# Optimization experiments

Hardware: AMD Instinct MI355X
Metric: run time of the kernel (lower is better)

Reference implementation:

```python
import jax, jax.numpy as jnp
import numpy as np

B, L, DM, H = 2, 2048, 512, 8
D = DM // H
FACTOR = 5
NUM_K = int(FACTOR * np.ceil(np.log(L)))  # 40
NUM_Q = NUM_K  # q_len == k_len here
EPS = 1e-5


def setup_inputs() -> dict:
    key = jax.random.key(0)
    ks = jax.random.split(key, 12)
    s = DM ** -0.5
    return {
        "q": jax.random.normal(ks[0], (B, L, DM), jnp.float32),
        "k": jax.random.normal(ks[1], (B, L, DM), jnp.float32),
        "v": jax.random.normal(ks[2], (B, L, DM), jnp.float32),
        "Wq": jax.random.normal(ks[3], (DM, DM), jnp.float32) * s,
        "bq": jnp.zeros((DM,), jnp.float32),
        "Wk": jax.random.normal(ks[4], (DM, DM), jnp.float32) * s,
        "bk": jnp.zeros((DM,), jnp.float32),
        "Wv": jax.random.normal(ks[5], (DM, DM), jnp.float32) * s,
        "bv": jnp.zeros((DM,), jnp.float32),
        "gamma": jnp.ones((DM,), jnp.float32),
        "beta": jnp.zeros((DM,), jnp.float32),
        "random_index": jax.random.randint(ks[6], (L, NUM_K), 0, L, jnp.int32),
    }


def _heads(x):
    # [B, L, DM] -> [B, H, L, D]
    return x.reshape(B, L, H, D).transpose(0, 2, 1, 3)


def reference(q, k, v, Wq, bq, Wk, bk, Wv, bv, gamma, beta, random_index):
    qp = _heads(q @ Wq + bq)
    kp = _heads(k @ Wk + bk)
    vp = _heads(v @ Wv + bv)

    # ProbSparse: sample NUM_K keys per query position (shared over batch/head)
    k_samp = kp[:, :, random_index, :]                      # [B,H,L,NUM_K,D]
    pre = jnp.einsum('bhid,bhijd->bhij', qp, k_samp)        # [B,H,L,NUM_K]
    measure = pre.max(-1) - pre.sum(-1) / L                 # sparsity measure [B,H,L]
    _, q_idx = jax.lax.top_k(measure, NUM_Q)                # [B,H,NUM_Q]

    q_sel = jnp.take_along_axis(qp, q_idx[..., None], axis=2)   # [B,H,NUM_Q,D]
    attn = jnp.einsum('bhid,bhjd->bhij', q_sel, kp) * D ** -0.5 # [B,H,NUM_Q,L]
    attn = jax.nn.softmax(attn, axis=-1)                    # dropout = identity (eval)
    out_sel = jnp.einsum('bhij,bhjd->bhid', attn, vp)       # [B,H,NUM_Q,D]

    # use_mask=False path: context is the mean of v over keys
    v_mean = vp.mean(axis=2)                                # [B,H,D]
    context = jnp.broadcast_to(v_mean[:, :, None, :], (B, H, L, D))
    bi = jnp.arange(B)[:, None, None]
    hi = jnp.arange(H)[None, :, None]
    out = context.at[bi, hi, q_idx].set(out_sel)            # scatter selected rows

    out = out.transpose(0, 2, 1, 3).reshape(B, L, DM)
    y = out + q
    mu = y.mean(-1, keepdims=True)
    var = y.var(-1, keepdims=True)
    yn = (y - mu) / jnp.sqrt(var + EPS) * gamma + beta
    return (yn, attn)
```

## Files before the change

kernel.cpp:

```cpp
#include <hip/hip_runtime.h>
#include <math.h>

#define BB 2
#define LL 2048
#define DMM 512
#define HH 8
#define DD 64
#define NUMK 40
#define NUMQ 40
#define LNEPS 1e-5f
#define LSEG 512
#define NLS 4

typedef unsigned short ushort_t;
typedef __attribute__((ext_vector_type(8))) short bf16x8;
typedef __attribute__((ext_vector_type(4))) float f32x4;

__device__ inline ushort_t f2bf(float x) {
    union { float f; unsigned int u; } v; v.f = x;
    unsigned int r = v.u + 0x7fffu + ((v.u >> 16) & 1u);
    return (ushort_t)(r >> 16);
}
__device__ inline float bf2f(ushort_t h) {
    union { unsigned int u; float f; } v; v.u = ((unsigned int)h) << 16;
    return v.f;
}

__global__ __launch_bounds__(256) void convert_x_kernel(
    const float* __restrict__ q, const float* __restrict__ k, const float* __restrict__ v,
    ushort_t* __restrict__ Xh, ushort_t* __restrict__ Xl) {
    const size_t plane = (size_t)BB * LL * DMM;
    const float* X = (blockIdx.y == 0) ? q : (blockIdx.y == 1) ? k : v;
    ushort_t* xh = Xh + plane * blockIdx.y;
    ushort_t* xl = Xl + plane * blockIdx.y;
    const size_t base = ((size_t)blockIdx.x * 256 + threadIdx.x) * 8;
    float4 a = *(const float4*)(X + base);
    float4 b = *(const float4*)(X + base + 4);
    float xs[8] = {a.x, a.y, a.z, a.w, b.x, b.y, b.z, b.w};
    unsigned int hp[4], lp[4];
#pragma unroll
    for (int j = 0; j < 4; ++j) {
        ushort_t h0 = f2bf(xs[2 * j]),     h1 = f2bf(xs[2 * j + 1]);
        ushort_t l0 = f2bf(xs[2 * j] - bf2f(h0));
        ushort_t l1 = f2bf(xs[2 * j + 1] - bf2f(h1));
        hp[j] = (unsigned int)h0 | ((unsigned int)h1 << 16);
        lp[j] = (unsigned int)l0 | ((unsigned int)l1 << 16);
    }
    *(uint4*)(xh + base) = make_uint4(hp[0], hp[1], hp[2], hp[3]);
    *(uint4*)(xl + base) = make_uint4(lp[0], lp[1], lp[2], lp[3]);
}

__global__ __launch_bounds__(256) void convert_w_kernel(
    const float* __restrict__ Wq, const float* __restrict__ Wk, const float* __restrict__ Wv,
    ushort_t* __restrict__ Wht, ushort_t* __restrict__ Wlt) {
    __shared__ float tile[64][65];
    const size_t plane = (size_t)DMM * DMM;
    const float* W = (blockIdx.z == 0) ? Wq : (blockIdx.z == 1) ? Wk : Wv;
    ushort_t* wht = Wht + plane * blockIdx.z;
    ushort_t* wlt = Wlt + plane * blockIdx.z;
    const int n0 = blockIdx.x * 64, k0 = blockIdx.y * 64;
    const int t = threadIdx.x;
    const int d = t & 63, g = t >> 6;
    for (int rr = g; rr < 64; rr += 4)
        tile[rr][d] = W[(size_t)(k0 + rr) * DMM + n0 + d];
    __syncthreads();
    for (int cc = g; cc < 64; cc += 4) {
        float x = tile[d][cc];
        ushort_t hi = f2bf(x);
        ushort_t lo = f2bf(x - bf2f(hi));
        wht[(size_t)(n0 + cc) * DMM + k0 + d] = hi;
        wlt[(size_t)(n0 + cc) * DMM + k0 + d] = lo;
    }
}

__device__ inline void stage_one(const ushort_t* __restrict__ g, ushort_t* lbuf,
                                 int r0, int lane, int k0) {
    const int r = r0 + (lane >> 3);
    const int c = (lane & 7) ^ (r & 7);
    const ushort_t* gp = g + (size_t)r * DMM + k0 + c * 8;
    __builtin_amdgcn_global_load_lds(
        (const __attribute__((address_space(1))) unsigned int*)gp,
        (__attribute__((address_space(3))) unsigned int*)(lbuf + (size_t)r0 * 64),
        16, 0, 0);
}
__device__ inline bf16x8 frag_ld(const ushort_t* buf, int row, int c) {
    const int idx = row * 8 + (c ^ (row & 7));
    return *(const bf16x8*)(buf + idx * 8);
}

__global__ __launch_bounds__(256, 2) void proj_mfma_kernel(
    const ushort_t* __restrict__ Xh, const ushort_t* __restrict__ Xl,
    const ushort_t* __restrict__ Wht, const ushort_t* __restrict__ Wlt,
    const float* __restrict__ bq, const float* __restrict__ bk, const float* __restrict__ bv,
    float* __restrict__ Oq, float* __restrict__ Ok, float* __restrict__ Ov) {
    const int z = blockIdx.z;
    const size_t xplane = (size_t)BB * LL * DMM;
    const size_t wplane = (size_t)DMM * DMM;
    const ushort_t* ah_g = Xh + xplane * z;
    const ushort_t* al_g = Xl + xplane * z;
    const ushort_t* bh_g = Wht + wplane * z;
    const ushort_t* bl_g = Wlt + wplane * z;
    const float* bias = (z == 0) ? bq : (z == 1) ? bk : bv;
    float* Out = (z == 0) ? Oq : (z == 1) ? Ok : Ov;

    __shared__ __align__(16) ushort_t bufAh[128 * 64];
    __shared__ __align__(16) ushort_t bufAl[128 * 64];
    __shared__ __align__(16) ushort_t bufBh[128 * 64];
    __shared__ __align__(16) ushort_t bufBl[128 * 64];

    const int t = threadIdx.x;
    const int lane = t & 63, w = t >> 6;
    const int wm = (w & 1) * 64, wn = (w >> 1) * 64;
    const int m0 = blockIdx.x * 128, j0 = blockIdx.y * 128;

    const ushort_t* A_h = ah_g + (size_t)m0 * DMM;
    const ushort_t* A_l = al_g + (size_t)m0 * DMM;
    const ushort_t* B_h = bh_g + (size_t)j0 * DMM;
    const ushort_t* B_l = bl_g + (size_t)j0 * DMM;

    f32x4 acc[4][4];
#pragma unroll
    for (int i = 0; i < 4; ++i)
#pragma unroll
        for (int j = 0; j < 4; ++j) acc[i][j] = (f32x4){0.f, 0.f, 0.f, 0.f};

    for (int ch = 0; ch < 8; ++ch) {
        const int k0 = ch * 64;
#pragma unroll
        for (int i = 0; i < 4; ++i) {
            const int r0 = (w * 4 + i) * 8;
            stage_one(A_h, bufAh, r0, lane, k0);
            stage_one(A_l, bufAl, r0, lane, k0);
            stage_one(B_h, bufBh, r0, lane, k0);
            stage_one(B_l, bufBl, r0, lane, k0);
        }
        __syncthreads();
#pragma unroll
        for (int ks = 0; ks < 2; ++ks) {
            const int cc = ks * 4 + (lane >> 4);
            bf16x8 fah[4], fal[4];
#pragma unroll
            for (int tm = 0; tm < 4; ++tm) {
                const int row = wm + tm * 16 + (lane & 15);
                fah[tm] = frag_ld(bufAh, row, cc);
                fal[tm] = frag_ld(bufAl, row, cc);
            }
#pragma unroll
            for (int tn = 0; tn < 4; ++tn) {
                const int rowb = wn + tn * 16 + (lane & 15);
                const bf16x8 fbh = frag_ld(bufBh, rowb, cc);
                const bf16x8 fbl = frag_ld(bufBl, rowb, cc);
#pragma unroll
                for (int tm = 0; tm < 4; ++tm) {
                    acc[tm][tn] = __builtin_amdgcn_mfma_f32_16x16x32_bf16(fah[tm], fbh, acc[tm][tn], 0, 0, 0);
                    acc[tm][tn] = __builtin_amdgcn_mfma_f32_16x16x32_bf16(fal[tm], fbh, acc[tm][tn], 0, 0, 0);
                    acc[tm][tn] = __builtin_amdgcn_mfma_f32_16x16x32_bf16(fah[tm], fbl, acc[tm][tn], 0, 0, 0);
                }
            }
        }
        __syncthreads();
    }

#pragma unroll
    for (int tn = 0; tn < 4; ++tn) {
        const int gn = j0 + wn + tn * 16 + (lane & 15);
        const float bvv = bias[gn];
        const int h = gn >> 6, d = gn & 63;
#pragma unroll
        for (int tm = 0; tm < 4; ++tm) {
#pragma unroll
            for (int reg = 0; reg < 4; ++reg) {
                const int gm = m0 + wm + tm * 16 + (lane >> 4) * 4 + reg;
                const int b = gm >> 11, l = gm & (LL - 1);
                Out[(((size_t)(b * HH + h)) * LL + l) * DD + d] = acc[tm][tn][reg] + bvv;
            }
        }
    }
}

__global__ __launch_bounds__(256) void measure_kernel(const float* __restrict__ qp2,
                                                      const float* __restrict__ kp2,
                                                      const int* __restrict__ rnd,
                                                      float* __restrict__ measure) {
    const int t = threadIdx.x;
    const int lane = t & 63;
    const int wv = t >> 6;
    const int g = lane >> 4;
    const int dq = (lane & 15) * 4;
    const int bh = blockIdx.x;
    const int i = blockIdx.y * 16 + wv * 4 + g;
    const float4 qv = *(const float4*)(qp2 + ((size_t)bh * LL + i) * DD + dq);
    const float* kbase = kp2 + (size_t)bh * LL * DD;
    const int* rp = rnd + i * NUMK;
    float mx = -INFINITY, sm = 0.f;
#pragma unroll 8
    for (int j = 0; j < NUMK; ++j) {
        const int row = rp[j];
        const float4 kv = *(const float4*)(kbase + (size_t)row * DD + dq);
        float p = kv.x * qv.x;
        p = fmaf(kv.y, qv.y, p); p = fmaf(kv.z, qv.z, p); p = fmaf(kv.w, qv.w, p);
        p += __shfl_xor(p, 1, 64);
        p += __shfl_xor(p, 2, 64);
        p += __shfl_xor(p, 4, 64);
        p += __shfl_xor(p, 8, 64);
        mx = fmaxf(mx, p);
        sm += p;
    }
    if ((lane & 15) == 0) measure[(size_t)bh * LL + i] = mx - sm * (1.0f / LL);
}

__global__ __launch_bounds__(256) void topk_kernel(const float* __restrict__ measure,
                                                   int* __restrict__ q_idx,
                                                   int* __restrict__ sel_pos) {
    __shared__ unsigned int keys[LL];
    __shared__ int hist[256];
    __shared__ unsigned int prefix_sh;
    __shared__ int need_sh;
    __shared__ unsigned int cval[256];
    __shared__ int cidx[256];
    __shared__ int cnt;
    const int t = threadIdx.x;
    const int bh = blockIdx.x;
    for (int i = t; i < LL; i += 256) {
        const float f = measure[(size_t)bh * LL + i];
        unsigned int u = __float_as_uint(f);
        keys[i] = (u & 0x80000000u) ? ~u : (u | 0x80000000u);
        sel_pos[(size_t)bh * LL + i] = -1;
    }
    if (t == 0) { prefix_sh = 0u; need_sh = NUMQ; cnt = 0; }
    __syncthreads();

    for (int round = 0; round < 4; ++round) {
        const int shift = 24 - round * 8;
        hist[t] = 0;
        __syncthreads();
        const unsigned int pref = prefix_sh;
        const unsigned int mask = (round == 0) ? 0u : (0xFFFFFFFFu << (shift + 8));
        for (int i = t; i < LL; i += 256) {
            const unsigned int key = keys[i];
            if ((key & mask) == pref)
                atomicAdd(&hist[(key >> shift) & 0xFF], 1);
        }
        __syncthreads();
        if (t == 0) {
            const int need = need_sh;
            int acc = 0;
            int v = 255;
            for (; v > 0; --v) {
                if (acc + hist[v] >= need) break;
                acc += hist[v];
            }
            need_sh = need - acc;
            prefix_sh = pref | ((unsigned int)v << shift);
        }
        __syncthreads();
    }
    const unsigned int K40 = prefix_sh;

    for (int i = t; i < LL; i += 256) {
        if (keys[i] >= K40) {
            int p = atomicAdd(&cnt, 1);
            if (p < 256) { cval[p] = keys[i]; cidx[p] = i; }
        }
    }
    __syncthreads();
    int M = cnt; if (M > 256) M = 256;
    for (int i = t; i < M; i += 256) {
        const unsigned int ki = cval[i];
        const int ii = cidx[i];
        int r = 0;
        for (int j = 0; j < M; ++j) {
            const unsigned int kj = cval[j];
            r += (kj > ki || (kj == ki && cidx[j] < ii)) ? 1 : 0;
        }
        if (r < NUMQ) {
            q_idx[bh * NUMQ + r] = ii;
            sel_pos[(size_t)bh * LL + ii] = r;
        }
    }
}

__global__ __launch_bounds__(256) void attn_part_kernel(
    const float* __restrict__ qp2, const float* __restrict__ kp2,
    const float* __restrict__ vp2, const int* __restrict__ q_idx,
    float* __restrict__ attn_out, float* __restrict__ part_m,
    float* __restrict__ part_s, float* __restrict__ part_pv) {
    __shared__ __align__(16) float buf[2][64 * 64];
    __shared__ __align__(16) float sc[4][LSEG];
    __shared__ float pvred[16][68];
    const int t = threadIdx.x;
    const int lane = t & 63, w = t >> 6;
    const int bh = blockIdx.x;
    const int qg = blockIdx.y;
    const int ls = blockIdx.z;
    const int l0 = ls * LSEG;
    const int dseg = lane >> 4;
    const int kk = lane & 15;

    float qrf[4][16];
#pragma unroll
    for (int qq = 0; qq < 4; ++qq) {
        const int qi = q_idx[bh * NUMQ + qg * 4 + qq];
        const float* qrow = qp2 + ((size_t)bh * LL + qi) * DD + dseg * 16;
#pragma unroll
        for (int j = 0; j < 4; ++j) {
            float4 v = *(const float4*)(qrow + j * 4);
            qrf[qq][j * 4 + 0] = v.x * 0.125f;
            qrf[qq][j * 4 + 1] = v.y * 0.125f;
            qrf[qq][j * 4 + 2] = v.z * 0.125f;
            qrf[qq][j * 4 + 3] = v.w * 0.125f;
        }
    }

    const float* kseg = kp2 + ((size_t)bh * LL + l0) * DD;
    const float* vseg = vp2 + ((size_t)bh * LL + l0) * DD;

    auto stage = [&](const float* gsrc, float* lb) {
#pragma unroll
        for (int i = 0; i < 4; ++i) {
            const int instr = w * 4 + i;
            const int r = instr * 4 + (lane >> 4);
            const int cg = (lane & 15) ^ (r & 15);
            const float* gp = gsrc + (size_t)r * DD + cg * 4;
            __builtin_amdgcn_global_load_lds(
                (const __attribute__((address_space(1))) unsigned int*)gp,
                (__attribute__((address_space(3))) unsigned int*)(lb + instr * 256),
                16, 0, 0);
        }
    };

    stage(kseg, buf[0]);
    const int krow = w * 16 + kk;
    for (int c = 0; c < 8; ++c) {
        __syncthreads();
        if (c < 7) stage(kseg + (size_t)(c + 1) * 64 * DD, buf[(c + 1) & 1]);
        const float* lb = buf[c & 1];
        float dot[4] = {0.f, 0.f, 0.f, 0.f};
#pragma unroll
        for (int j = 0; j < 4; ++j) {
            const int cg = dseg * 4 + j;
            const float4 k4 = *(const float4*)(lb + krow * 64 + ((cg ^ (krow & 15)) * 4));
            const float kf[4] = {k4.x, k4.y, k4.z, k4.w};
#pragma unroll
            for (int qq = 0; qq < 4; ++qq)
#pragma unroll
                for (int m = 0; m < 4; ++m)
                    dot[qq] = fmaf(qrf[qq][j * 4 + m], kf[m], dot[qq]);
        }
#pragma unroll
        for (int qq = 0; qq < 4; ++qq) {
            dot[qq] += __shfl_xor(dot[qq], 16, 64);
            dot[qq] += __shfl_xor(dot[qq], 32, 64);
        }
        const float sel = (dseg == 0) ? dot[0] : (dseg == 1) ? dot[1]
                        : (dseg == 2) ? dot[2] : dot[3];
        sc[dseg][c * 64 + krow] = sel;
    }
    stage(vseg, buf[0]);
    __syncthreads();

    const int row = bh * NUMQ + qg * 4 + w;
    {
        float* srow = sc[w];
        float4 v0 = *(float4*)(srow + lane * 8);
        float4 v1 = *(float4*)(srow + lane * 8 + 4);
        float m = fmaxf(fmaxf(fmaxf(v0.x, v0.y), fmaxf(v0.z, v0.w)),
                        fmaxf(fmaxf(v1.x, v1.y), fmaxf(v1.z, v1.w)));
#pragma unroll
        for (int off = 32; off > 0; off >>= 1) m = fmaxf(m, __shfl_xor(m, off, 64));
        v0.x = __expf(v0.x - m); v0.y = __expf(v0.y - m);
        v0.z = __expf(v0.z - m); v0.w = __expf(v0.w - m);
        v1.x = __expf(v1.x - m); v1.y = __expf(v1.y - m);
        v1.z = __expf(v1.z - m); v1.w = __expf(v1.w - m);
        *(float4*)(srow + lane * 8) = v0;
        *(float4*)(srow + lane * 8 + 4) = v1;
        float* arow = attn_out + (size_t)row * LL + l0;
        *(float4*)(arow + lane * 8) = v0;
        *(float4*)(arow + lane * 8 + 4) = v1;
        float s = (v0.x + v0.y + v0.z + v0.w) + (v1.x + v1.y + v1.z + v1.w);
#pragma unroll
        for (int off = 32; off > 0; off >>= 1) s += __shfl_xor(s, off, 64);
        if (lane == 0) {
            part_m[row * NLS + ls] = m;
            part_s[row * NLS + ls] = s;
        }
    }

    const int dq4 = (t & 15) * 4;
    const int grp = t >> 4;
    float4 acc[4];
#pragma unroll
    for (int qq = 0; qq < 4; ++qq) acc[qq] = make_float4(0.f, 0.f, 0.f, 0.f);
    for (int c = 0; c < 8; ++c) {
        __syncthreads();
        if (c < 7) stage(vseg + (size_t)(c + 1) * 64 * DD, buf[(c + 1) & 1]);
        const float* lb = buf[c & 1];
        float pa[4][4];
#pragma unroll
        for (int qq = 0; qq < 4; ++qq)
            *(float4*)&pa[qq][0] = *(const float4*)&sc[qq][c * 64 + grp * 4];
#pragma unroll
        for (int i = 0; i < 4; ++i) {
            const int r = grp * 4 + i;
            const float4 v4 = *(const float4*)(lb + r * 64 + (((t & 15) ^ (r & 15)) * 4));
#pragma unroll
            for (int qq = 0; qq < 4; ++qq) {
                acc[qq].x = fmaf(pa[qq][i], v4.x, acc[qq].x);
                acc[qq].y = fmaf(pa[qq][i], v4.y, acc[qq].y);
                acc[qq].z = fmaf(pa[qq][i], v4.z, acc[qq].z);
                acc[qq].w = fmaf(pa[qq][i], v4.w, acc[qq].w);
            }
        }
    }
#pragma unroll
    for (int qq = 0; qq < 4; ++qq) {
        __syncthreads();
        *(float4*)&pvred[grp][dq4] = acc[qq];
        __syncthreads();
        if (t < DD) {
            float s = 0.f;
#pragma unroll
            for (int u = 0; u < 16; ++u) s += pvred[u][t];
            const int prow = bh * NUMQ + qg * 4 + qq;
            part_pv[((size_t)prow * NLS + ls) * DD + t] = s;
        }
    }
}

__global__ __launch_bounds__(256) void attn_fin_kernel(
    const float* __restrict__ part_m, const float* __restrict__ part_s,
    const float* __restrict__ part_pv, float* __restrict__ attn_out,
    float* __restrict__ out_sel) {
    const int row = blockIdx.x;
    const int t = threadIdx.x;
    float m0 = part_m[row * NLS + 0], m1 = part_m[row * NLS + 1];
    float m2 = part_m[row * NLS + 2], m3 = part_m[row * NLS + 3];
    float M = fmaxf(fmaxf(m0, m1), fmaxf(m2, m3));
    float f[NLS];
    f[0] = __expf(m0 - M); f[1] = __expf(m1 - M);
    f[2] = __expf(m2 - M); f[3] = __expf(m3 - M);
    float T = part_s[row * NLS + 0] * f[0] + part_s[row * NLS + 1] * f[1]
            + part_s[row * NLS + 2] * f[2] + part_s[row * NLS + 3] * f[3];
    const float inv = 1.0f / T;
    float* arow = attn_out + (size_t)row * LL;
    {
        float4 v0 = *(const float4*)&arow[4 * t];
        float4 v1 = *(const float4*)&arow[1024 + 4 * t];
        const float g0 = f[(4 * t) >> 9] * inv;
        const float g1 = f[(1024 + 4 * t) >> 9] * inv;
        v0.x *= g0; v0.y *= g0; v0.z *= g0; v0.w *= g0;
        v1.x *= g1; v1.y *= g1; v1.z *= g1; v1.w *= g1;
        *(float4*)&arow[4 * t] = v0;
        *(float4*)&arow[1024 + 4 * t] = v1;
    }
    if (t < DD) {
        float s = part_pv[((size_t)row * NLS + 0) * DD + t] * f[0]
                + part_pv[((size_t)row * NLS + 1) * DD + t] * f[1]
                + part_pv[((size_t)row * NLS + 2) * DD + t] * f[2]
                + part_pv[((size_t)row * NLS + 3) * DD + t] * f[3];
        out_sel[(size_t)row * DD + t] = s * inv;
    }
}

__global__ __launch_bounds__(256) void vmean1_kernel(const float* __restrict__ vp2,
                                                     float* __restrict__ partial) {
    __shared__ float pv[256];
    const int t = threadIdx.x;
    const int chunk = blockIdx.x & 31;
    const int bh = blockIdx.x >> 5;
    const int d = t & 63, g = t >> 6;
    const int l0 = chunk * 64;
    float acc = 0.f;
    for (int l = l0 + g; l < l0 + 64; l += 4)
        acc += vp2[((size_t)bh * LL + l) * DD + d];
    pv[t] = acc;
    __syncthreads();
    if (t < 64)
        partial[(size_t)blockIdx.x * 64 + t] = pv[t] + pv[64 + t] + pv[128 + t] + pv[192 + t];
}

__global__ __launch_bounds__(64) void vmean2_kernel(const float* __restrict__ partial,
                                                    float* __restrict__ v_mean) {
    const int bh = blockIdx.x;
    const int t = threadIdx.x;
    float s = 0.f;
    for (int c = 0; c < 32; ++c)
        s += partial[((size_t)bh * 32 + c) * 64 + t];
    v_mean[bh * 64 + t] = s * (1.0f / LL);
}

__global__ __launch_bounds__(512) void final_kernel(const float* __restrict__ q_in,
                                                    const int* __restrict__ sel_pos,
                                                    const float* __restrict__ out_sel,
                                                    const float* __restrict__ v_mean,
                                                    const float* __restrict__ gamma,
                                                    const float* __restrict__ beta,
                                                    float* __restrict__ yout) {
    __shared__ float wred[8];
    const int j = threadIdx.x;
    const int lane = j & 63, wv = j >> 6;
    const int tok = blockIdx.x;
    const int b = tok >> 11;
    const int l = tok & (LL - 1);
    const int h = wv, d = lane;
    const int bh = b * HH + h;
    const int p = sel_pos[(size_t)bh * LL + l];
    float val = (p >= 0) ? out_sel[((size_t)bh * NUMQ + p) * DD + d]
                         : v_mean[bh * DD + d];
    float y = val + q_in[(size_t)tok * DMM + j];
    float s = y;
#pragma unroll
    for (int off = 32; off > 0; off >>= 1) s += __shfl_xor(s, off, 64);
    if (lane == 0) wred[wv] = s;
    __syncthreads();
    float tot = 0.f;
#pragma unroll
    for (int u = 0; u < 8; ++u) tot += wred[u];
    float mu = tot * (1.0f / DMM);
    __syncthreads();
    float dv = y - mu;
    float s2 = dv * dv;
#pragma unroll
    for (int off = 32; off > 0; off >>= 1) s2 += __shfl_xor(s2, off, 64);
    if (lane == 0) wred[wv] = s2;
    __syncthreads();
    float tot2 = 0.f;
#pragma unroll
    for (int u = 0; u < 8; ++u) tot2 += wred[u];
    float var = tot2 * (1.0f / DMM);
    float yn = dv * rsqrtf(var + LNEPS) * gamma[j] + beta[j];
    yout[(size_t)tok * DMM + j] = yn;
}

extern "C" void kernel_launch(void* const* d_in, const int* in_sizes, int n_in,
                              void* d_out, int out_size, void* d_ws, size_t ws_size,
                              hipStream_t stream) {
    const float* q     = (const float*)d_in[0];
    const float* k     = (const float*)d_in[1];
    const float* v     = (const float*)d_in[2];
    const float* Wq    = (const float*)d_in[3];
    const float* bq    = (const float*)d_in[4];
    const float* Wk    = (const float*)d_in[5];
    const float* bk    = (const float*)d_in[6];
    const float* Wv    = (const float*)d_in[7];
    const float* bv    = (const float*)d_in[8];
    const float* gamma = (const float*)d_in[9];
    const float* beta  = (const float*)d_in[10];
    const int*   rnd   = (const int*)d_in[11];

    float* ws = (float*)d_ws;
    const size_t proj_sz = (size_t)BB * HH * LL * DD;
    float* qp2     = ws;
    float* kp2     = qp2 + proj_sz;
    float* vp2     = kp2 + proj_sz;
    float* measure = vp2 + proj_sz;
    float* out_sel = measure + (size_t)BB * HH * LL;
    float* v_mean  = out_sel + (size_t)BB * HH * NUMQ * DD;
    float* partial = v_mean + (size_t)BB * HH * DD;
    float* part_m  = partial + (size_t)BB * HH * 32 * 64;
    float* part_s  = part_m + (size_t)BB * HH * NUMQ * NLS;
    float* part_pv = part_s + (size_t)BB * HH * NUMQ * NLS;
    int*   q_idx   = (int*)(part_pv + (size_t)BB * HH * NUMQ * NLS * DD);
    int*   sel_pos = q_idx + BB * HH * NUMQ;
    ushort_t* Xh  = (ushort_t*)(sel_pos + BB * HH * LL);
    ushort_t* Xl  = Xh + 3 * proj_sz;
    ushort_t* Wht = Xl + 3 * proj_sz;
    ushort_t* Wlt = Wht + 3 * (size_t)DMM * DMM;

    float* yn_out   = (float*)d_out;
    float* attn_out = yn_out + (size_t)BB * LL * DMM;

    convert_x_kernel<<<dim3(BB * LL * DMM / (256 * 8), 3), 256, 0, stream>>>(q, k, v, Xh, Xl);
    convert_w_kernel<<<dim3(DMM / 64, DMM / 64, 3), 256, 0, stream>>>(Wq, Wk, Wv, Wht, Wlt);
    proj_mfma_kernel<<<dim3(BB * LL / 128, DMM / 128, 3), 256, 0, stream>>>(
        Xh, Xl, Wht, Wlt, bq, bk, bv, qp2, kp2, vp2);
    vmean1_kernel<<<BB * HH * 32, 256, 0, stream>>>(vp2, partial);
    vmean2_kernel<<<BB * HH, 64, 0, stream>>>(partial, v_mean);
    measure_kernel<<<dim3(BB * HH, LL / 16), 256, 0, stream>>>(qp2, kp2, rnd, measure);
    topk_kernel<<<BB * HH, 256, 0, stream>>>(measure, q_idx, sel_pos);
    attn_part_kernel<<<dim3(BB * HH, NUMQ / 4, NLS), 256, 0, stream>>>(
        qp2, kp2, vp2, q_idx, attn_out, part_m, part_s, part_pv);
    attn_fin_kernel<<<BB * HH * NUMQ, 256, 0, stream>>>(
        part_m, part_s, part_pv, attn_out, out_sel);
    final_kernel<<<BB * LL, 512, 0, stream>>>(q, sel_pos, out_sel, v_mean, gamma, beta, yn_out);
}
```

Before: 217.9 us.

## Restructure attention partials so each block handles all queries over shorter key segments

The attention partial kernel now processes all 40 selected queries per block over 128-key segments (16 segments), staging K and V once into LDS and reusing them across every query. Before, it used 4-query groups over 512-key segments, so K and V were reloaded ten times per head. The finalize kernel is generalized to merge 16 partials. Separately, the projection GEMM grid is flattened into one dimension with a remapped block order, which may improve L2 locality across the XCDs. The cost is more partial results to merge and larger LDS use per block.

```diff
diff --git a/kernel.cpp b/kernel.cpp
--- a/kernel.cpp
+++ b/kernel.cpp
@@ -9,8 +9,8 @@
 #define NUMK 40
 #define NUMQ 40
 #define LNEPS 1e-5f
-#define LSEG 512
-#define NLS 4
+#define LSEG 128
+#define NLS 16
 
 typedef unsigned short ushort_t;
 typedef __attribute__((ext_vector_type(8))) short bf16x8;
@@ -93,7 +93,10 @@
     const ushort_t* __restrict__ Wht, const ushort_t* __restrict__ Wlt,
     const float* __restrict__ bq, const float* __restrict__ bk, const float* __restrict__ bv,
     float* __restrict__ Oq, float* __restrict__ Ok, float* __restrict__ Ov) {
-    const int z = blockIdx.z;
+    const int orig = blockIdx.x;
+    const int c = (orig & 7) * 48 + (orig >> 3);
+    const int jb = c & 3, mb = (c >> 2) & 31, z = c >> 7;
+
     const size_t xplane = (size_t)BB * LL * DMM;
     const size_t wplane = (size_t)DMM * DMM;
     const ushort_t* ah_g = Xh + xplane * z;
@@ -111,7 +114,7 @@
     const int t = threadIdx.x;
     const int lane = t & 63, w = t >> 6;
     const int wm = (w & 1) * 64, wn = (w >> 1) * 64;
-    const int m0 = blockIdx.x * 128, j0 = blockIdx.y * 128;
+    const int m0 = mb * 128, j0 = jb * 128;
 
     const ushort_t* A_h = ah_g + (size_t)m0 * DMM;
     const ushort_t* A_l = al_g + (size_t)m0 * DMM;
@@ -285,145 +288,126 @@
     const float* __restrict__ vp2, const int* __restrict__ q_idx,
     float* __restrict__ attn_out, float* __restrict__ part_m,
     float* __restrict__ part_s, float* __restrict__ part_pv) {
-    __shared__ __align__(16) float buf[2][64 * 64];
-    __shared__ __align__(16) float sc[4][LSEG];
-    __shared__ float pvred[16][68];
+    __shared__ __align__(16) float Qs[NUMQ][68];
+    __shared__ __align__(16) float Ks[LSEG * 64];
+    __shared__ __align__(16) float Vs[LSEG * 64];
+    __shared__ __align__(16) float Ss[NUMQ][136];
     const int t = threadIdx.x;
     const int lane = t & 63, w = t >> 6;
     const int bh = blockIdx.x;
-    const int qg = blockIdx.y;
-    const int ls = blockIdx.z;
+    const int ls = blockIdx.y;
     const int l0 = ls * LSEG;
-    const int dseg = lane >> 4;
-    const int kk = lane & 15;
-
-    float qrf[4][16];
-#pragma unroll
-    for (int qq = 0; qq < 4; ++qq) {
-        const int qi = q_idx[bh * NUMQ + qg * 4 + qq];
-        const float* qrow = qp2 + ((size_t)bh * LL + qi) * DD + dseg * 16;
-#pragma unroll
-        for (int j = 0; j < 4; ++j) {
-            float4 v = *(const float4*)(qrow + j * 4);
-            qrf[qq][j * 4 + 0] = v.x * 0.125f;
-            qrf[qq][j * 4 + 1] = v.y * 0.125f;
-            qrf[qq][j * 4 + 2] = v.z * 0.125f;
-            qrf[qq][j * 4 + 3] = v.w * 0.125f;
-        }
+
+    for (int idx = t; idx < NUMQ * 16; idx += 256) {
+        const int r = idx >> 4, c4 = idx & 15;
+        const int qi = q_idx[bh * NUMQ + r];
+        float4 v = *(const float4*)(qp2 + ((size_t)bh * LL + qi) * DD + c4 * 4);
+        Qs[r][c4 * 4 + 0] = v.x * 0.125f;
+        Qs[r][c4 * 4 + 1] = v.y * 0.125f;
+        Qs[r][c4 * 4 + 2] = v.z * 0.125f;
+        Qs[r][c4 * 4 + 3] = v.w * 0.125f;
     }
 
     const float* kseg = kp2 + ((size_t)bh * LL + l0) * DD;
     const float* vseg = vp2 + ((size_t)bh * LL + l0) * DD;
-
-    auto stage = [&](const float* gsrc, float* lb) {
-#pragma unroll
-        for (int i = 0; i < 4; ++i) {
-            const int instr = w * 4 + i;
-            const int r = instr * 4 + (lane >> 4);
-            const int cg = (lane & 15) ^ (r & 15);
-            const float* gp = gsrc + (size_t)r * DD + cg * 4;
-            __builtin_amdgcn_global_load_lds(
-                (const __attribute__((address_space(1))) unsigned int*)gp,
-                (__attribute__((address_space(3))) unsigned int*)(lb + instr * 256),
-                16, 0, 0);
-        }
-    };
-
-    stage(kseg, buf[0]);
-    const int krow = w * 16 + kk;
-    for (int c = 0; c < 8; ++c) {
-        __syncthreads();
-        if (c < 7) stage(kseg + (size_t)(c + 1) * 64 * DD, buf[(c + 1) & 1]);
-        const float* lb = buf[c & 1];
-        float dot[4] = {0.f, 0.f, 0.f, 0.f};
-#pragma unroll
-        for (int j = 0; j < 4; ++j) {
-            const int cg = dseg * 4 + j;
-            const float4 k4 = *(const float4*)(lb + krow * 64 + ((cg ^ (krow & 15)) * 4));
-            const float kf[4] = {k4.x, k4.y, k4.z, k4.w};
-#pragma unroll
-            for (int qq = 0; qq < 4; ++qq)
-#pragma unroll
-                for (int m = 0; m < 4; ++m)
-                    dot[qq] = fmaf(qrf[qq][j * 4 + m], kf[m], dot[qq]);
-        }
-#pragma unroll
-        for (int qq = 0; qq < 4; ++qq) {
-            dot[qq] += __shfl_xor(dot[qq], 16, 64);
-            dot[qq] += __shfl_xor(dot[qq], 32, 64);
-        }
-        const float sel = (dseg == 0) ? dot[0] : (dseg == 1) ? dot[1]
-                        : (dseg == 2) ? dot[2] : dot[3];
-        sc[dseg][c * 64 + krow] = sel;
-    }
-    stage(vseg, buf[0]);
-    __syncthreads();
-
-    const int row = bh * NUMQ + qg * 4 + w;
-    {
-        float* srow = sc[w];
-        float4 v0 = *(float4*)(srow + lane * 8);
-        float4 v1 = *(float4*)(srow + lane * 8 + 4);
-        float m = fmaxf(fmaxf(fmaxf(v0.x, v0.y), fmaxf(v0.z, v0.w)),
-                        fmaxf(fmaxf(v1.x, v1.y), fmaxf(v1.z, v1.w)));
-#pragma unroll
-        for (int off = 32; off > 0; off >>= 1) m = fmaxf(m, __shfl_xor(m, off, 64));
-        v0.x = __expf(v0.x - m); v0.y = __expf(v0.y - m);
-        v0.z = __expf(v0.z - m); v0.w = __expf(v0.w - m);
-        v1.x = __expf(v1.x - m); v1.y = __expf(v1.y - m);
-        v1.z = __expf(v1.z - m); v1.w = __expf(v1.w - m);
-        *(float4*)(srow + lane * 8) = v0;
-        *(float4*)(srow + lane * 8 + 4) = v1;
-        float* arow = attn_out + (size_t)row * LL + l0;
-        *(float4*)(arow + lane * 8) = v0;
-        *(float4*)(arow + lane * 8 + 4) = v1;
-        float s = (v0.x + v0.y + v0.z + v0.w) + (v1.x + v1.y + v1.z + v1.w);
-#pragma unroll
-        for (int off = 32; off > 0; off >>= 1) s += __shfl_xor(s, off, 64);
-        if (lane == 0) {
+#pragma unroll
+    for (int i = 0; i < 8; ++i) {
+        const int r0 = (w * 8 + i) * 4;
+        const int r = r0 + (lane >> 4);
+        const int cg = (lane & 15) ^ (r & 15);
+        __builtin_amdgcn_global_load_lds(
+            (const __attribute__((address_space(1))) unsigned int*)(kseg + (size_t)r * DD + cg * 4),
+            (__attribute__((address_space(3))) unsigned int*)(Ks + r0 * 64), 16, 0, 0);
+        __builtin_amdgcn_global_load_lds(
+            (const __attribute__((address_space(1))) unsigned int*)(vseg + (size_t)r * DD + cg * 4),
+            (__attribute__((address_space(3))) unsigned int*)(Vs + r0 * 64), 16, 0, 0);
+    }
+    __syncthreads();
+
+    const int qt = t >> 5;
+    const int jt = t & 31;
+    float acc[5][4];
+#pragma unroll
+    for (int i = 0; i < 5; ++i)
+#pragma unroll
+        for (int jj = 0; jj < 4; ++jj) acc[i][jj] = 0.f;
+
+    for (int c4 = 0; c4 < 16; ++c4) {
+        float4 q4[5];
+#pragma unroll
+        for (int i = 0; i < 5; ++i)
+            q4[i] = *(const float4*)&Qs[qt + 8 * i][c4 * 4];
+#pragma unroll
+        for (int jj = 0; jj < 4; ++jj) {
+            const int r = jt + 32 * jj;
+            const float4 k4 = *(const float4*)&Ks[r * 64 + ((c4 ^ (r & 15)) * 4)];
+#pragma unroll
+            for (int i = 0; i < 5; ++i) {
+                acc[i][jj] = fmaf(q4[i].x, k4.x, acc[i][jj]);
+                acc[i][jj] = fmaf(q4[i].y, k4.y, acc[i][jj]);
+                acc[i][jj] = fmaf(q4[i].z, k4.z, acc[i][jj]);
+                acc[i][jj] = fmaf(q4[i].w, k4.w, acc[i][jj]);
+            }
+        }
+    }
+
+#pragma unroll
+    for (int i = 0; i < 5; ++i) {
+        const int r = qt + 8 * i;
+        float m = fmaxf(fmaxf(acc[i][0], acc[i][1]), fmaxf(acc[i][2], acc[i][3]));
+        m = fmaxf(m, __shfl_xor(m, 16, 64));
+        m = fmaxf(m, __shfl_xor(m, 8, 64));
+        m = fmaxf(m, __shfl_xor(m, 4, 64));
+        m = fmaxf(m, __shfl_xor(m, 2, 64));
+        m = fmaxf(m, __shfl_xor(m, 1, 64));
+        float p0 = __expf(acc[i][0] - m), p1 = __expf(acc[i][1] - m);
+        float p2 = __expf(acc[i][2] - m), p3 = __expf(acc[i][3] - m);
+        Ss[r][jt]      = p0;
+        Ss[r][jt + 32] = p1;
+        Ss[r][jt + 64] = p2;
+        Ss[r][jt + 96] = p3;
+        float s = p0 + p1 + p2 + p3;
+        s += __shfl_xor(s, 16, 64);
+        s += __shfl_xor(s, 8, 64);
+        s += __shfl_xor(s, 4, 64);
+        s += __shfl_xor(s, 2, 64);
+        s += __shfl_xor(s, 1, 64);
+        if (jt == 0) {
+            const int row = bh * NUMQ + r;
             part_m[row * NLS + ls] = m;
             part_s[row * NLS + ls] = s;
         }
     }
-
-    const int dq4 = (t & 15) * 4;
-    const int grp = t >> 4;
-    float4 acc[4];
-#pragma unroll
-    for (int qq = 0; qq < 4; ++qq) acc[qq] = make_float4(0.f, 0.f, 0.f, 0.f);
-    for (int c = 0; c < 8; ++c) {
-        __syncthreads();
-        if (c < 7) stage(vseg + (size_t)(c + 1) * 64 * DD, buf[(c + 1) & 1]);
-        const float* lb = buf[c & 1];
-        float pa[4][4];
-#pragma unroll
-        for (int qq = 0; qq < 4; ++qq)
-            *(float4*)&pa[qq][0] = *(const float4*)&sc[qq][c * 64 + grp * 4];
-#pragma unroll
-        for (int i = 0; i < 4; ++i) {
-            const int r = grp * 4 + i;
-            const float4 v4 = *(const float4*)(lb + r * 64 + (((t & 15) ^ (r & 15)) * 4));
-#pragma unroll
-            for (int qq = 0; qq < 4; ++qq) {
-                acc[qq].x = fmaf(pa[qq][i], v4.x, acc[qq].x);
-                acc[qq].y = fmaf(pa[qq][i], v4.y, acc[qq].y);
-                acc[qq].z = fmaf(pa[qq][i], v4.z, acc[qq].z);
-                acc[qq].w = fmaf(pa[qq][i], v4.w, acc[qq].w);
-            }
-        }
-    }
-#pragma unroll
-    for (int qq = 0; qq < 4; ++qq) {
-        __syncthreads();
-        *(float4*)&pvred[grp][dq4] = acc[qq];
-        __syncthreads();
-        if (t < DD) {
-            float s = 0.f;
-#pragma unroll
-            for (int u = 0; u < 16; ++u) s += pvred[u][t];
-            const int prow = bh * NUMQ + qg * 4 + qq;
-            part_pv[((size_t)prow * NLS + ls) * DD + t] = s;
-        }
+    __syncthreads();
+
+    for (int idx = t; idx < NUMQ * 32; idx += 256) {
+        const int r = idx >> 5, c4 = idx & 31;
+        const float4 v = *(const float4*)&Ss[r][c4 * 4];
+        *(float4*)(attn_out + (size_t)(bh * NUMQ + r) * LL + l0 + c4 * 4) = v;
+    }
+
+    const int dt = t & 31;
+    float o[5][2];
+#pragma unroll
+    for (int i = 0; i < 5; ++i) { o[i][0] = 0.f; o[i][1] = 0.f; }
+#pragma unroll 4
+    for (int j = 0; j < LSEG; ++j) {
+        const int pg = (dt >> 1) ^ (j & 15);
+        const float* vr = &Vs[j * 64 + pg * 4 + (dt & 1) * 2];
+        const float v0 = vr[0], v1 = vr[1];
+#pragma unroll
+        for (int i = 0; i < 5; ++i) {
+            const float p = Ss[qt + 8 * i][j];
+            o[i][0] = fmaf(p, v0, o[i][0]);
+            o[i][1] = fmaf(p, v1, o[i][1]);
+        }
+    }
+#pragma unroll
+    for (int i = 0; i < 5; ++i) {
+        const int row = bh * NUMQ + qt + 8 * i;
+        float* pp = part_pv + ((size_t)row * NLS + ls) * DD + dt * 2;
+        pp[0] = o[i][0];
+        pp[1] = o[i][1];
     }
 }
 
@@ -433,31 +417,31 @@
     float* __restrict__ out_sel) {
     const int row = blockIdx.x;
     const int t = threadIdx.x;
-    float m0 = part_m[row * NLS + 0], m1 = part_m[row * NLS + 1];
-    float m2 = part_m[row * NLS + 2], m3 = part_m[row * NLS + 3];
-    float M = fmaxf(fmaxf(m0, m1), fmaxf(m2, m3));
-    float f[NLS];
-    f[0] = __expf(m0 - M); f[1] = __expf(m1 - M);
-    f[2] = __expf(m2 - M); f[3] = __expf(m3 - M);
-    float T = part_s[row * NLS + 0] * f[0] + part_s[row * NLS + 1] * f[1]
-            + part_s[row * NLS + 2] * f[2] + part_s[row * NLS + 3] * f[3];
+    float M = -INFINITY;
+#pragma unroll
+    for (int i = 0; i < NLS; ++i) M = fmaxf(M, part_m[row * NLS + i]);
+    float T = 0.f;
+#pragma unroll
+    for (int i = 0; i < NLS; ++i)
+        T += part_s[row * NLS + i] * __expf(part_m[row * NLS + i] - M);
     const float inv = 1.0f / T;
     float* arow = attn_out + (size_t)row * LL;
     {
+        const int s0 = t >> 5;
+        const float g0 = __expf(part_m[row * NLS + s0] - M) * inv;
+        const float g1 = __expf(part_m[row * NLS + 8 + s0] - M) * inv;
         float4 v0 = *(const float4*)&arow[4 * t];
         float4 v1 = *(const float4*)&arow[1024 + 4 * t];
-        const float g0 = f[(4 * t) >> 9] * inv;
-        const float g1 = f[(1024 + 4 * t) >> 9] * inv;
         v0.x *= g0; v0.y *= g0; v0.z *= g0; v0.w *= g0;
         v1.x *= g1; v1.y *= g1; v1.z *= g1; v1.w *= g1;
         *(float4*)&arow[4 * t] = v0;
         *(float4*)&arow[1024 + 4 * t] = v1;
     }
     if (t < DD) {
-        float s = part_pv[((size_t)row * NLS + 0) * DD + t] * f[0]
-                + part_pv[((size_t)row * NLS + 1) * DD + t] * f[1]
-                + part_pv[((size_t)row * NLS + 2) * DD + t] * f[2]
-                + part_pv[((size_t)row * NLS + 3) * DD + t] * f[3];
+        float s = 0.f;
+#pragma unroll
+        for (int i = 0; i < NLS; ++i)
+            s += part_pv[((size_t)row * NLS + i) * DD + t] * __expf(part_m[row * NLS + i] - M);
         out_sel[(size_t)row * DD + t] = s * inv;
     }
 }
@@ -572,13 +556,13 @@
 
     convert_x_kernel<<<dim3(BB * LL * DMM / (256 * 8), 3), 256, 0, stream>>>(q, k, v, Xh, Xl);
     convert_w_kernel<<<dim3(DMM / 64, DMM / 64, 3), 256, 0, stream>>>(Wq, Wk, Wv, Wht, Wlt);
-    proj_mfma_kernel<<<dim3(BB * LL / 128, DMM / 128, 3), 256, 0, stream>>>(
+    proj_mfma_kernel<<<dim3(3 * (BB * LL / 128) * (DMM / 128), 1, 1), 256, 0, stream>>>(
         Xh, Xl, Wht, Wlt, bq, bk, bv, qp2, kp2, vp2);
     vmean1_kernel<<<BB * HH * 32, 256, 0, stream>>>(vp2, partial);
     vmean2_kernel<<<BB * HH, 64, 0, stream>>>(partial, v_mean);
     measure_kernel<<<dim3(BB * HH, LL / 16), 256, 0, stream>>>(qp2, kp2, rnd, measure);
     topk_kernel<<<BB * HH, 256, 0, stream>>>(measure, q_idx, sel_pos);
-    attn_part_kernel<<<dim3(BB * HH, NUMQ / 4, NLS), 256, 0, stream>>>(
+    attn_part_kernel<<<dim3(BB * HH, NLS), 256, 0, stream>>>(
         qp2, kp2, vp2, q_idx, attn_out, part_m, part_s, part_pv);
     attn_fin_kernel<<<BB * HH * NUMQ, 256, 0, stream>>>(
         part_m, part_s, part_pv, attn_out, out_sel);
```

New measurement: 213.8 us. About the same (-1.9%).
